# Kernel tuning notes

Hardware: AMD Instinct MI355X
Metric: run time of the kernel (lower is better)

Reference implementation:

```python
import jax, jax.numpy as jnp
import numpy as np

B, N, C, H, K = 16, 1024, 384, 6, 8
HID = int(C * 2.0)  # mlp_ratio = 2.0
HD = C // H


def _layernorm(x, w, b, eps=1e-5):
    m = x.mean(-1, keepdims=True)
    v = ((x - m) ** 2).mean(-1, keepdims=True)
    return (x - m) * jax.lax.rsqrt(v + eps) * w + b


def setup_inputs() -> dict:
    key = jax.random.key(0)
    ks = jax.random.split(key, 16)
    x = jax.random.normal(ks[0], (B, N, C), jnp.float32)
    # knn indices within each batch, offset by batch*N (as in get_knn_index)
    idx = jax.random.randint(ks[1], (B, K, N), 0, N)
    base = jnp.arange(B, dtype=jnp.int32)[:, None, None] * N
    knn_index = (idx + base).reshape(-1).astype(jnp.int32)
    s = 0.02
    p = {
        "x": x,
        "knn_index": knn_index,
        "ln1_w": jnp.ones((C,), jnp.float32),
        "ln1_b": jnp.zeros((C,), jnp.float32),
        "w_qkv": jax.random.normal(ks[2], (C, 3 * C), jnp.float32) * s,  # qkv_bias=False
        "w_proj": jax.random.normal(ks[3], (C, C), jnp.float32) * s,
        "b_proj": jnp.zeros((C,), jnp.float32),
        "w_knn": jax.random.normal(ks[4], (2 * C, C), jnp.float32) * s,
        "b_knn": jnp.zeros((C,), jnp.float32),
        "w_merge": jax.random.normal(ks[5], (2 * C, C), jnp.float32) * s,
        "b_merge": jnp.zeros((C,), jnp.float32),
        "ln2_w": jnp.ones((C,), jnp.float32),
        "ln2_b": jnp.zeros((C,), jnp.float32),
        "w_fc1": jax.random.normal(ks[6], (C, HID), jnp.float32) * s,
        "b_fc1": jnp.zeros((HID,), jnp.float32),
        "w_fc2": jax.random.normal(ks[7], (HID, C), jnp.float32) * s,
        "b_fc2": jnp.zeros((C,), jnp.float32),
    }
    return p


def reference(x, knn_index, ln1_w, ln1_b, w_qkv, w_proj, b_proj, w_knn, b_knn,
              w_merge, b_merge, ln2_w, ln2_b, w_fc1, b_fc1, w_fc2, b_fc2):
    nx = _layernorm(x, ln1_w, ln1_b)  # [B,N,C]

    # --- self attention ---
    qkv = (nx @ w_qkv).reshape(B, N, 3, H, HD)
    q, k, v = qkv[:, :, 0], qkv[:, :, 1], qkv[:, :, 2]  # [B,N,H,HD]
    scale = HD ** (-0.5)
    attn = jnp.einsum("bnhd,bmhd->bhnm", q, k) * scale
    attn = jax.nn.softmax(attn, axis=-1)
    a_out = jnp.einsum("bhnm,bmhd->bnhd", attn, v).reshape(B, N, C)
    x1 = a_out @ w_proj + b_proj

    # --- graph feature: gather, relative concat, Linear+LeakyReLU, max over k ---
    feat = nx.reshape(B * N, C)[knn_index].reshape(B, K, N, C)
    center = nx[:, None, :, :]  # [B,1,N,C]
    g = jnp.concatenate([feat - center, jnp.broadcast_to(center, (B, K, N, C))], axis=-1)
    knn_f = jax.nn.leaky_relu(g @ w_knn + b_knn, negative_slope=0.2)
    knn_f = knn_f.max(axis=1)  # [B,N,C]

    x1 = jnp.concatenate([x1, knn_f], axis=-1) @ w_merge + b_merge
    x = x + x1

    # --- MLP ---
    h = _layernorm(x, ln2_w, ln2_b)
    h = jax.nn.gelu(h @ w_fc1 + b_fc1, approximate=False) @ w_fc2 + b_fc2
    return x + h
```

## Files before the change

kernel.cpp:

```cpp
#include <hip/hip_runtime.h>
#include <hip/hip_bf16.h>
#include <math.h>

#define BN_ROWS 16384
#define CDIM 384
#define NH 6
#define BBATCH 16
#define NNN 1024

typedef unsigned short u16;
typedef unsigned int u32;
typedef __attribute__((ext_vector_type(8))) short short8;
typedef __attribute__((ext_vector_type(4))) float floatx4;

__device__ __forceinline__ float b2f(u16 s) { return __uint_as_float(((u32)s) << 16); }
__device__ __forceinline__ u16 f2b(float f) {
    __hip_bfloat16 h = __float2bfloat16(f);
    u16 s; __builtin_memcpy(&s, &h, 2); return s;
}
__device__ __forceinline__ u32 cvt_pk_bf16(float lo, float hi) {
    u32 r;
    asm("v_cvt_pk_bf16_f32 %0, %1, %2" : "=v"(r) : "v"(lo), "v"(hi));
    return r;
}
__device__ __forceinline__ void gload_lds16(const u16* g, u16* l) {
    __builtin_amdgcn_global_load_lds(
        (const __attribute__((address_space(1))) unsigned int*)g,
        (__attribute__((address_space(3))) unsigned int*)l, 16, 0, 0);
}

__global__ __launch_bounds__(256) void pack_all(
    const float* __restrict__ W0, u16* __restrict__ T0,
    const float* __restrict__ W1, u16* __restrict__ T1,
    const float* __restrict__ W2, u16* __restrict__ T2,
    const float* __restrict__ W3, u16* __restrict__ T3,
    const float* __restrict__ W4, u16* __restrict__ T4,
    const float* __restrict__ W5, u16* __restrict__ T5)
{
    const float* W; u16* T; int K, N;
    switch (blockIdx.z) {
        case 0: W = W0; T = T0; K = 384; N = 1152; break;
        case 1: W = W1; T = T1; K = 384; N = 384;  break;
        case 2: W = W2; T = T2; K = 768; N = 384;  break;
        case 3: W = W3; T = T3; K = 768; N = 384;  break;
        case 4: W = W4; T = T4; K = 384; N = 768;  break;
        default: W = W5; T = T5; K = 768; N = 384; break;
    }
    const int n0 = blockIdx.x * 32, k0 = blockIdx.y * 32;
    if (n0 >= N || k0 >= K) return;
    __shared__ float s[32][33];
    const int tx = threadIdx.x & 31, ty = threadIdx.x >> 5;
#pragma unroll
    for (int i = 0; i < 4; ++i)
        s[ty + 8 * i][tx] = W[(size_t)(k0 + ty + 8 * i) * N + n0 + tx];
    __syncthreads();
#pragma unroll
    for (int i = 0; i < 4; ++i)
        T[(size_t)(n0 + ty + 8 * i) * K + k0 + tx] = f2b(s[tx][ty + 8 * i]);
}

__global__ __launch_bounds__(64) void ln_kernel(const float* __restrict__ xin,
                                                const float* __restrict__ w,
                                                const float* __restrict__ b,
                                                u16* __restrict__ out)
{
    const int row = blockIdx.x;
    const int t = threadIdx.x;
    const size_t base = (size_t)row * CDIM;
    float v[6];
#pragma unroll
    for (int i = 0; i < 6; ++i) v[i] = xin[base + t + 64 * i];
    float s = 0.f, s2 = 0.f;
#pragma unroll
    for (int i = 0; i < 6; ++i) { s += v[i]; s2 += v[i] * v[i]; }
#pragma unroll
    for (int m = 1; m < 64; m <<= 1) {
        s  += __shfl_xor(s,  m, 64);
        s2 += __shfl_xor(s2, m, 64);
    }
    const float mean = s * (1.0f / CDIM);
    const float var  = s2 * (1.0f / CDIM) - mean * mean;
    const float rs   = rsqrtf(var + 1e-5f);
#pragma unroll
    for (int i = 0; i < 6; ++i) {
        int c = t + 64 * i;
        out[base + c] = f2b((v[i] - mean) * rs * w[c] + b[c]);
    }
}

template<int ACT, bool HAS_BIAS, bool HAS_RES, bool OUT_F32, int MODE, int NT, bool SWZ>
__global__ __launch_bounds__(256) void gemm_mfma_kernel(
    const u16* __restrict__ A, int lda,
    const u16* __restrict__ Bt, const u16* __restrict__ Bt2, int ldbt,
    u16* Cb, u16* Cb2, u16* Cb3, float* Cf, int ldc,
    const float* __restrict__ bias,
    const float* res,
    int K)
{
    constexpr int NTL = NT / 32;
    __shared__ u16 As[2][128 * 32];
    __shared__ u16 Bs[2][NT * 32];
    const int tid  = threadIdx.x;
    const int wv   = tid >> 6;
    const int lane = tid & 63;
    const int l15  = lane & 15;
    const int quad = lane >> 4;

    int m0, n0;
    if (SWZ) {
        const int nbx = gridDim.x;
        const int total = nbx * gridDim.y;
        int lin = blockIdx.x + nbx * blockIdx.y;
        const int cpx = total >> 3;
        lin = (lin & 7) * cpx + (lin >> 3);
        m0 = (lin / nbx) * 128;
        n0 = (lin % nbx) * NT;
    } else {
        m0 = blockIdx.y * 128;
        n0 = blockIdx.x * NT;
    }

    const int woffm = (wv >> 1) * 64;
    const int woffn = (wv & 1) * (NT / 2);

    const u16* bsrc; int brow0, koff, bld;
    if constexpr (MODE == 3) {
        if (n0 < 1152)      { bsrc = Bt;  brow0 = n0;        koff = 0;   bld = 384; }
        else if (n0 < 1536) { bsrc = Bt2; brow0 = n0 - 1152; koff = 0;   bld = 768; }
        else                { bsrc = Bt2; brow0 = n0 - 1536; koff = 384; bld = 768; }
    } else {
        bsrc  = (MODE == 2 && n0 >= 384) ? Bt2 : Bt;
        brow0 = (MODE == 2 && n0 >= 384) ? (n0 - 384) : n0;
        koff = 0; bld = ldbt;
    }

    floatx4 acc[4][NTL];
#pragma unroll
    for (int mt = 0; mt < 4; ++mt)
#pragma unroll
        for (int nt = 0; nt < NTL; ++nt) acc[mt][nt] = (floatx4){0.f, 0.f, 0.f, 0.f};

    const int gsw  = 8 * ((lane & 3) ^ ((lane >> 3) & 3));
    const int rloc = lane >> 2;
    const int rdsw = 8 * (quad ^ ((l15 >> 1) & 3));

    auto stage = [&](int kt, int p) {
#pragma unroll
        for (int j = 0; j < 2; ++j) {
            const int slab = 32 * wv + 16 * j;
            gload_lds16(A + (size_t)(m0 + slab + rloc) * lda + kt + gsw, &As[p][slab * 32]);
        }
        if (NT == 128) {
#pragma unroll
            for (int j = 0; j < 2; ++j) {
                const int slab = 32 * wv + 16 * j;
                gload_lds16(bsrc + (size_t)(brow0 + slab + rloc) * bld + koff + kt + gsw,
                            &Bs[p][slab * 32]);
            }
        } else {
            const int slab = 16 * wv;
            gload_lds16(bsrc + (size_t)(brow0 + slab + rloc) * bld + koff + kt + gsw,
                        &Bs[p][slab * 32]);
        }
    };

    stage(0, 0);
    stage(32, 1);
    int cur = 0;
    for (int kt = 0; kt < K; kt += 32) {
        if (kt + 32 < K) {
            if constexpr (NT == 128) asm volatile("s_waitcnt vmcnt(4)" ::: "memory");
            else                     asm volatile("s_waitcnt vmcnt(3)" ::: "memory");
        } else {
            asm volatile("s_waitcnt vmcnt(0)" ::: "memory");
        }
        __builtin_amdgcn_sched_barrier(0);
        __builtin_amdgcn_s_barrier();
        __builtin_amdgcn_sched_barrier(0);

        short8 af[4], bf[NTL];
#pragma unroll
        for (int mt = 0; mt < 4; ++mt)
            af[mt] = *(const short8*)(As[cur] + (woffm + mt * 16 + l15) * 32 + rdsw);
#pragma unroll
        for (int nt = 0; nt < NTL; ++nt)
            bf[nt] = *(const short8*)(Bs[cur] + (woffn + nt * 16 + l15) * 32 + rdsw);
#pragma unroll
        for (int mt = 0; mt < 4; ++mt)
#pragma unroll
            for (int nt = 0; nt < NTL; ++nt)
                acc[mt][nt] = __builtin_amdgcn_mfma_f32_16x16x32_bf16(
                    bf[nt], af[mt], acc[mt][nt], 0, 0, 0);
        __builtin_amdgcn_sched_barrier(0);
        __builtin_amdgcn_s_barrier();
        __builtin_amdgcn_sched_barrier(0);
        if (kt + 64 < K) stage(kt + 64, cur);
        cur ^= 1;
    }

#pragma unroll
    for (int mt = 0; mt < 4; ++mt) {
        const int gr = m0 + woffm + mt * 16 + l15;
#pragma unroll
        for (int nt = 0; nt < NTL; ++nt) {
            const int gc0 = n0 + woffn + nt * 16 + quad * 4;
            float v4[4];
#pragma unroll
            for (int rr = 0; rr < 4; ++rr) v4[rr] = acc[mt][nt][rr];
            if (HAS_BIAS) {
                const floatx4 bv = *(const floatx4*)(bias + gc0);
#pragma unroll
                for (int rr = 0; rr < 4; ++rr) v4[rr] += bv[rr];
            }
            if (MODE == 2 && gc0 >= 384) {
                const floatx4 bv = *(const floatx4*)(bias + gc0 - 384);
#pragma unroll
                for (int rr = 0; rr < 4; ++rr) v4[rr] += bv[rr];
            }
            if (MODE == 3 && gc0 >= 1536) {
                const floatx4 bv = *(const floatx4*)(bias + gc0 - 1536);
#pragma unroll
                for (int rr = 0; rr < 4; ++rr) v4[rr] += bv[rr];
            }
            if (ACT == 1) {
#pragma unroll
                for (int rr = 0; rr < 4; ++rr)
                    v4[rr] = 0.5f * v4[rr] * (1.0f + erff(v4[rr] * 0.70710678118654752f));
            }
            if (HAS_RES) {
                const floatx4 rv = *(const floatx4*)(res + (size_t)gr * ldc + gc0);
#pragma unroll
                for (int rr = 0; rr < 4; ++rr) v4[rr] += rv[rr];
            }
            if (MODE == 1 || (MODE == 3 && gc0 < 1152)) {
                const int t3  = gc0 / 384;
                const int rem = gc0 - t3 * 384;
                const int hh = rem >> 6, dd = rem & 63;
                const int bb = gr >> 10, nn = gr & 1023;
                u32 lo = cvt_pk_bf16(v4[0], v4[1]);
                u32 hi = cvt_pk_bf16(v4[2], v4[3]);
                *(uint2*)(Cb + ((size_t)((bb * 6 + hh) * 1024 + nn)) * 192 + t3 * 64 + dd) =
                    make_uint2(lo, hi);
            } else if (MODE == 3) {
                u32 lo = cvt_pk_bf16(v4[0], v4[1]);
                u32 hi = cvt_pk_bf16(v4[2], v4[3]);
                if (gc0 < 1536)
                    *(uint2*)(Cb2 + (size_t)gr * 384 + gc0 - 1152) = make_uint2(lo, hi);
                else
                    *(uint2*)(Cb3 + (size_t)gr * 384 + gc0 - 1536) = make_uint2(lo, hi);
            } else if (MODE == 2) {
                u32 lo = cvt_pk_bf16(v4[0], v4[1]);
                u32 hi = cvt_pk_bf16(v4[2], v4[3]);
                if (gc0 < 384)
                    *(uint2*)(Cb  + (size_t)gr * 384 + gc0)       = make_uint2(lo, hi);
                else
                    *(uint2*)(Cb2 + (size_t)gr * 384 + gc0 - 384) = make_uint2(lo, hi);
            } else if (OUT_F32) {
                floatx4 vv = {v4[0], v4[1], v4[2], v4[3]};
                *(floatx4*)(Cf + (size_t)gr * ldc + gc0) = vv;
            } else {
                u32 lo = cvt_pk_bf16(v4[0], v4[1]);
                u32 hi = cvt_pk_bf16(v4[2], v4[3]);
                *(uint2*)(Cb + (size_t)gr * ldc + gc0) = make_uint2(lo, hi);
            }
        }
    }
}

__global__ __launch_bounds__(256) void attn_mfma_kernel(const u16* __restrict__ qkv2,
                                                        u16* __restrict__ aout)
{
    const int id = blockIdx.x;
    const int rxcd = id & 7;
    const int j = id >> 3;
    const int slab = rxcd + 8 * (j % 12);
    const int qtile = j / 12;
    const int b = slab / NH, h = slab % NH;

    const int wave = threadIdx.x >> 6;
    const int lane = threadIdx.x & 63;
    const int l15 = lane & 15;
    const int quad = lane >> 4;
    const int qbase = qtile * 128 + wave * 32;
    const int tid = threadIdx.x;

    const u16* slabp = qkv2 + ((size_t)(b * NH + h) << 10) * 192;

    __shared__ __align__(16) u16 Ks[64 * 72];
    __shared__ __align__(16) u16 Vt[64 * 72];
    __shared__ __align__(16) u16 Ps[4][32 * 72];

    short8 qf[2][2];
#pragma unroll
    for (int nt = 0; nt < 2; ++nt) {
        const u16* qrow = slabp + (size_t)(qbase + nt * 16 + l15) * 192;
        qf[nt][0] = *(const short8*)(qrow + quad * 8);
        qf[nt][1] = *(const short8*)(qrow + 32 + quad * 8);
    }

    short8 vones;
#pragma unroll
    for (int i = 0; i < 8; ++i) vones[i] = (l15 == 0) ? (short)0x3F80 : (short)0;

    floatx4 Oacc[2][4];
    floatx4 rAcc[2];
#pragma unroll
    for (int mt = 0; mt < 2; ++mt) {
        rAcc[mt] = (floatx4){0.f, 0.f, 0.f, 0.f};
#pragma unroll
        for (int nt = 0; nt < 4; ++nt) Oacc[mt][nt] = (floatx4){0.f, 0.f, 0.f, 0.f};
    }

    const int key = tid >> 2, dblk = (tid & 3) * 16;
    const int kp2 = tid & 31, db = (tid >> 5) * 8;
    uint4 kr0, kr1, vr0, vr1;
    {
        const u16* kp = slabp + (size_t)key * 192 + 64 + dblk;
        kr0 = *(const uint4*)(kp);
        kr1 = *(const uint4*)(kp + 8);
        const u16* vp = slabp + (size_t)(2 * kp2) * 192 + 128 + db;
        vr0 = *(const uint4*)(vp);
        vr1 = *(const uint4*)(vp + 192);
    }

    for (int kc = 0; kc < NNN; kc += 64) {
        *(uint4*)(Ks + key * 72 + dblk)     = kr0;
        *(uint4*)(Ks + key * 72 + dblk + 8) = kr1;
        {
            u32 a0[4] = {vr0.x, vr0.y, vr0.z, vr0.w};
            u32 a1[4] = {vr1.x, vr1.y, vr1.z, vr1.w};
#pragma unroll
            for (int i = 0; i < 4; ++i) {
                u32 lo = __builtin_amdgcn_perm(a1[i], a0[i], 0x05040100u);
                u32 hi = __builtin_amdgcn_perm(a1[i], a0[i], 0x07060302u);
                *(u32*)(Vt + (size_t)(db + 2 * i)     * 72 + 2 * kp2) = lo;
                *(u32*)(Vt + (size_t)(db + 2 * i + 1) * 72 + 2 * kp2) = hi;
            }
        }
        __syncthreads();

        if (kc + 64 < NNN) {
            const u16* kp = slabp + (size_t)(kc + 64 + key) * 192 + 64 + dblk;
            kr0 = *(const uint4*)(kp);
            kr1 = *(const uint4*)(kp + 8);
            const u16* vp = slabp + (size_t)(kc + 64 + 2 * kp2) * 192 + 128 + db;
            vr0 = *(const uint4*)(vp);
            vr1 = *(const uint4*)(vp + 192);
        }

        floatx4 sc[4][2];
        __builtin_amdgcn_s_setprio(1);
#pragma unroll
        for (int kt_ = 0; kt_ < 4; ++kt_) {
            short8 kf0 = *(const short8*)(Ks + (kt_ * 16 + l15) * 72 + quad * 8);
            short8 kf1 = *(const short8*)(Ks + (kt_ * 16 + l15) * 72 + 32 + quad * 8);
#pragma unroll
            for (int nt = 0; nt < 2; ++nt) {
                floatx4 s = {0.f, 0.f, 0.f, 0.f};
                s = __builtin_amdgcn_mfma_f32_16x16x32_bf16(kf0, qf[nt][0], s, 0, 0, 0);
                s = __builtin_amdgcn_mfma_f32_16x16x32_bf16(kf1, qf[nt][1], s, 0, 0, 0);
                sc[kt_][nt] = s;
            }
        }
        __builtin_amdgcn_s_setprio(0);

#pragma unroll
        for (int kt_ = 0; kt_ < 4; ++kt_)
#pragma unroll
            for (int nt = 0; nt < 2; ++nt) {
                float pv[4];
#pragma unroll
                for (int rr = 0; rr < 4; ++rr)
                    pv[rr] = __expf(sc[kt_][nt][rr] * 0.125f);
                u32 lo = cvt_pk_bf16(pv[0], pv[1]);
                u32 hi = cvt_pk_bf16(pv[2], pv[3]);
                *(uint2*)(Ps[wave] + (nt * 16 + l15) * 72 + kt_ * 16 + quad * 4) =
                    make_uint2(lo, hi);
            }

        short8 pf[2][2];
#pragma unroll
        for (int mt = 0; mt < 2; ++mt) {
            pf[mt][0] = *(const short8*)(Ps[wave] + (mt * 16 + l15) * 72 + quad * 8);
            pf[mt][1] = *(const short8*)(Ps[wave] + (mt * 16 + l15) * 72 + 32 + quad * 8);
        }
        __builtin_amdgcn_s_setprio(1);
#pragma unroll
        for (int mt = 0; mt < 2; ++mt) {
            rAcc[mt] = __builtin_amdgcn_mfma_f32_16x16x32_bf16(pf[mt][0], vones, rAcc[mt], 0, 0, 0);
            rAcc[mt] = __builtin_amdgcn_mfma_f32_16x16x32_bf16(pf[mt][1], vones, rAcc[mt], 0, 0, 0);
        }
#pragma unroll
        for (int nt = 0; nt < 4; ++nt) {
#pragma unroll
            for (int kk = 0; kk < 2; ++kk) {
                short8 vf = *(const short8*)(Vt + (size_t)(nt * 16 + l15) * 72 + kk * 32 + quad * 8);
#pragma unroll
                for (int mt = 0; mt < 2; ++mt)
                    Oacc[mt][nt] = __builtin_amdgcn_mfma_f32_16x16x32_bf16(
                        pf[mt][kk], vf, Oacc[mt][nt], 0, 0, 0);
            }
        }
        __builtin_amdgcn_s_setprio(0);
        __syncthreads();
    }

#pragma unroll
    for (int mt = 0; mt < 2; ++mt) {
#pragma unroll
        for (int rr = 0; rr < 4; ++rr) {
            float l = __shfl(rAcc[mt][rr], quad << 4, 64);
            float inv = 1.0f / l;
            int q = qbase + mt * 16 + quad * 4 + rr;
#pragma unroll
            for (int nt = 0; nt < 4; ++nt)
                aout[(size_t)(b * NNN + q) * CDIM + h * 64 + nt * 16 + l15] =
                    f2b(Oacc[mt][nt][rr] * inv);
        }
    }
}

__global__ __launch_bounds__(128) void knnmax_kernel(const u16* __restrict__ t1,
                                                     const u16* __restrict__ t2,
                                                     const int* __restrict__ idx,
                                                     u16* __restrict__ x1cat)
{
    const int bn = blockIdx.x * 2 + (threadIdx.x >> 6);
    const int lane = threadIdx.x & 63;
    if (lane >= 48) return;
    const int b = bn >> 10, n = bn & 1023;
    int ind[8];
#pragma unroll
    for (int k = 0; k < 8; ++k) ind[k] = idx[b * 8192 + k * 1024 + n];
    const int c0 = lane * 8;
    const size_t rbase = (size_t)bn * CDIM + c0;
    short8 v1 = *(const short8*)(t1 + rbase);
    short8 v2 = *(const short8*)(t2 + rbase);
    float basef[8], mx[8];
#pragma unroll
    for (int j = 0; j < 8; ++j) {
        basef[j] = b2f((u16)v2[j]) - b2f((u16)v1[j]);
        mx[j] = -1e30f;
    }
#pragma unroll
    for (int k = 0; k < 8; ++k) {
        short8 nv = *(const short8*)(t1 + (size_t)ind[k] * CDIM + c0);
#pragma unroll
        for (int j = 0; j < 8; ++j) {
            float v = b2f((u16)nv[j]) + basef[j];
            v = (v > 0.f) ? v : 0.2f * v;
            mx[j] = fmaxf(mx[j], v);
        }
    }
    short8 ov;
#pragma unroll
    for (int j = 0; j < 8; ++j) ov[j] = (short)f2b(mx[j]);
    *(short8*)(x1cat + (size_t)bn * 768 + CDIM + c0) = ov;
}

extern "C" void kernel_launch(void* const* d_in, const int* in_sizes, int n_in,
                              void* d_out, int out_size, void* d_ws, size_t ws_size,
                              hipStream_t stream)
{
    (void)in_sizes; (void)n_in; (void)out_size; (void)ws_size;
    const float* x     = (const float*)d_in[0];
    const int*   knn   = (const int*)d_in[1];
    const float* ln1w  = (const float*)d_in[2];
    const float* ln1b  = (const float*)d_in[3];
    const float* wqkv  = (const float*)d_in[4];
    const float* wproj = (const float*)d_in[5];
    const float* bproj = (const float*)d_in[6];
    const float* wknn  = (const float*)d_in[7];
    const float* bknn  = (const float*)d_in[8];
    const float* wmrg  = (const float*)d_in[9];
    const float* bmrg  = (const float*)d_in[10];
    const float* ln2w  = (const float*)d_in[11];
    const float* ln2b  = (const float*)d_in[12];
    const float* wfc1  = (const float*)d_in[13];
    const float* bfc1  = (const float*)d_in[14];
    const float* wfc2  = (const float*)d_in[15];
    const float* bfc2  = (const float*)d_in[16];

    u16* wsb = (u16*)d_ws;
    const size_t RE = (size_t)BN_ROWS * CDIM;
    u16* nxb   = wsb;
    u16* qkvb  = wsb + RE;
    u16* aoutb = wsb;
    u16* x1cat = wsb + RE;
    u16* hinb  = wsb;
    u16* h1b   = wsb + RE;
    u16* t1b   = (u16*)d_out;
    u16* t2b   = (u16*)d_out + RE;
    float* xmid = (float*)d_out;
    u16* wqkvT  = wsb + 4 * RE;
    u16* wprojT = wqkvT + 442368;
    u16* wknnT  = wprojT + 147456;
    u16* wmrgT  = wknnT + 294912;
    u16* wfc1T  = wmrgT + 294912;
    u16* wfc2T  = wfc1T + 294912;

    pack_all<<<dim3(36, 24, 6), 256, 0, stream>>>(
        wqkv, wqkvT, wproj, wprojT, wknn, wknnT, wmrg, wmrgT, wfc1, wfc1T, wfc2, wfc2T);
    ln_kernel<<<BN_ROWS, 64, 0, stream>>>(x, ln1w, ln1b, nxb);
    gemm_mfma_kernel<0, false, false, false, 3, 128, true><<<dim3(15, 128), 256, 0, stream>>>(
        nxb, CDIM, wqkvT, wknnT, 384, qkvb, t1b, t2b, nullptr, 0, bknn, nullptr, CDIM);
    attn_mfma_kernel<<<768, 256, 0, stream>>>(qkvb, aoutb);
    gemm_mfma_kernel<0, true, false, false, 0, 64, true><<<dim3(6, 128), 256, 0, stream>>>(
        aoutb, CDIM, wprojT, nullptr, CDIM, x1cat, nullptr, nullptr, nullptr, 768, bproj, nullptr, CDIM);
    knnmax_kernel<<<BN_ROWS / 2, 128, 0, stream>>>(t1b, t2b, knn, x1cat);
    gemm_mfma_kernel<0, true, true, true, 0, 64, true><<<dim3(6, 128), 256, 0, stream>>>(
        x1cat, 768, wmrgT, nullptr, 768, nullptr, nullptr, nullptr, xmid, CDIM, bmrg, x, 768);
    ln_kernel<<<BN_ROWS, 64, 0, stream>>>(xmid, ln2w, ln2b, hinb);
    gemm_mfma_kernel<1, true, false, false, 0, 128, true><<<dim3(6, 128), 256, 0, stream>>>(
        hinb, CDIM, wfc1T, nullptr, CDIM, h1b, nullptr, nullptr, nullptr, 768, bfc1, nullptr, CDIM);
    gemm_mfma_kernel<0, true, true, true, 0, 64, true><<<dim3(6, 128), 256, 0, stream>>>(
        h1b, 768, wfc2T, nullptr, 768, nullptr, nullptr, nullptr, (float*)d_out, CDIM, bfc2, xmid, 768);
}
```

Measured before the change: 306.1 us.

## Load GEMM MFMA fragments directly from global memory, dropping LDS staging

Result: slower. 498.2 us (+62.8%).

```diff
diff --git a/kernel.cpp b/kernel.cpp
--- a/kernel.cpp
+++ b/kernel.cpp
@@ -22,11 +22,6 @@
     u32 r;
     asm("v_cvt_pk_bf16_f32 %0, %1, %2" : "=v"(r) : "v"(lo), "v"(hi));
     return r;
-}
-__device__ __forceinline__ void gload_lds16(const u16* g, u16* l) {
-    __builtin_amdgcn_global_load_lds(
-        (const __attribute__((address_space(1))) unsigned int*)g,
-        (__attribute__((address_space(3))) unsigned int*)l, 16, 0, 0);
 }
 
 __global__ __launch_bounds__(256) void pack_all(
@@ -98,8 +93,6 @@
     int K)
 {
     constexpr int NTL = NT / 32;
-    __shared__ u16 As[2][128 * 32];
-    __shared__ u16 Bs[2][NT * 32];
     const int tid  = threadIdx.x;
     const int wv   = tid >> 6;
     const int lane = tid & 63;
@@ -140,63 +133,38 @@
 #pragma unroll
         for (int nt = 0; nt < NTL; ++nt) acc[mt][nt] = (floatx4){0.f, 0.f, 0.f, 0.f};
 
-    const int gsw  = 8 * ((lane & 3) ^ ((lane >> 3) & 3));
-    const int rloc = lane >> 2;
-    const int rdsw = 8 * (quad ^ ((l15 >> 1) & 3));
-
-    auto stage = [&](int kt, int p) {
-#pragma unroll
-        for (int j = 0; j < 2; ++j) {
-            const int slab = 32 * wv + 16 * j;
-            gload_lds16(A + (size_t)(m0 + slab + rloc) * lda + kt + gsw, &As[p][slab * 32]);
-        }
-        if (NT == 128) {
-#pragma unroll
-            for (int j = 0; j < 2; ++j) {
-                const int slab = 32 * wv + 16 * j;
-                gload_lds16(bsrc + (size_t)(brow0 + slab + rloc) * bld + koff + kt + gsw,
-                            &Bs[p][slab * 32]);
-            }
-        } else {
-            const int slab = 16 * wv;
-            gload_lds16(bsrc + (size_t)(brow0 + slab + rloc) * bld + koff + kt + gsw,
-                        &Bs[p][slab * 32]);
-        }
-    };
-
-    stage(0, 0);
-    stage(32, 1);
-    int cur = 0;
-    for (int kt = 0; kt < K; kt += 32) {
-        if (kt + 32 < K) {
-            if constexpr (NT == 128) asm volatile("s_waitcnt vmcnt(4)" ::: "memory");
-            else                     asm volatile("s_waitcnt vmcnt(3)" ::: "memory");
-        } else {
-            asm volatile("s_waitcnt vmcnt(0)" ::: "memory");
-        }
-        __builtin_amdgcn_sched_barrier(0);
-        __builtin_amdgcn_s_barrier();
-        __builtin_amdgcn_sched_barrier(0);
-
-        short8 af[4], bf[NTL];
-#pragma unroll
-        for (int mt = 0; mt < 4; ++mt)
-            af[mt] = *(const short8*)(As[cur] + (woffm + mt * 16 + l15) * 32 + rdsw);
-#pragma unroll
-        for (int nt = 0; nt < NTL; ++nt)
-            bf[nt] = *(const short8*)(Bs[cur] + (woffn + nt * 16 + l15) * 32 + rdsw);
-#pragma unroll
-        for (int mt = 0; mt < 4; ++mt)
-#pragma unroll
-            for (int nt = 0; nt < NTL; ++nt)
-                acc[mt][nt] = __builtin_amdgcn_mfma_f32_16x16x32_bf16(
-                    bf[nt], af[mt], acc[mt][nt], 0, 0, 0);
-        __builtin_amdgcn_sched_barrier(0);
-        __builtin_amdgcn_s_barrier();
-        __builtin_amdgcn_sched_barrier(0);
-        if (kt + 64 < K) stage(kt + 64, cur);
-        cur ^= 1;
-    }
+    const u16* Ab = A    + (size_t)(m0 + woffm + l15) * lda + quad * 8;
+    const u16* Bb = bsrc + (size_t)(brow0 + woffn + l15) * bld + koff + quad * 8;
+
+#define LDFRAG(kt, af, bf)                                                       \
+    {                                                                            \
+        _Pragma("unroll")                                                        \
+        for (int mt = 0; mt < 4; ++mt)                                           \
+            af[mt] = *(const short8*)(Ab + (size_t)mt * 16 * lda + (kt));        \
+        _Pragma("unroll")                                                        \
+        for (int nt = 0; nt < NTL; ++nt)                                         \
+            bf[nt] = *(const short8*)(Bb + (size_t)nt * 16 * bld + (kt));        \
+    }
+#define DOMFMA(af, bf)                                                           \
+    {                                                                            \
+        _Pragma("unroll")                                                        \
+        for (int mt = 0; mt < 4; ++mt)                                           \
+            _Pragma("unroll")                                                    \
+            for (int nt = 0; nt < NTL; ++nt)                                     \
+                acc[mt][nt] = __builtin_amdgcn_mfma_f32_16x16x32_bf16(           \
+                    bf[nt], af[mt], acc[mt][nt], 0, 0, 0);                       \
+    }
+
+    short8 af0[4], bf0[NTL], af1[4], bf1[NTL];
+    LDFRAG(0, af0, bf0);
+    for (int kt = 0; kt < K; kt += 64) {
+        LDFRAG(kt + 32, af1, bf1);
+        DOMFMA(af0, bf0);
+        if (kt + 64 < K) LDFRAG(kt + 64, af0, bf0);
+        DOMFMA(af1, bf1);
+    }
+#undef LDFRAG
+#undef DOMFMA
 
 #pragma unroll
     for (int mt = 0; mt < 4; ++mt) {
@@ -502,7 +470,7 @@
     pack_all<<<dim3(36, 24, 6), 256, 0, stream>>>(
         wqkv, wqkvT, wproj, wprojT, wknn, wknnT, wmrg, wmrgT, wfc1, wfc1T, wfc2, wfc2T);
     ln_kernel<<<BN_ROWS, 64, 0, stream>>>(x, ln1w, ln1b, nxb);
-    gemm_mfma_kernel<0, false, false, false, 3, 128, true><<<dim3(15, 128), 256, 0, stream>>>(
+    gemm_mfma_kernel<0, false, false, false, 3, 64, true><<<dim3(30, 128), 256, 0, stream>>>(
         nxb, CDIM, wqkvT, wknnT, 384, qkvb, t1b, t2b, nullptr, 0, bknn, nullptr, CDIM);
     attn_mfma_kernel<<<768, 256, 0, stream>>>(qkvb, aoutb);
     gemm_mfma_kernel<0, true, false, false, 0, 64, true><<<dim3(6, 128), 256, 0, stream>>>(
@@ -511,7 +479,7 @@
     gemm_mfma_kernel<0, true, true, true, 0, 64, true><<<dim3(6, 128), 256, 0, stream>>>(
         x1cat, 768, wmrgT, nullptr, 768, nullptr, nullptr, nullptr, xmid, CDIM, bmrg, x, 768);
     ln_kernel<<<BN_ROWS, 64, 0, stream>>>(xmid, ln2w, ln2b, hinb);
-    gemm_mfma_kernel<1, true, false, false, 0, 128, true><<<dim3(6, 128), 256, 0, stream>>>(
+    gemm_mfma_kernel<1, true, false, false, 0, 64, true><<<dim3(12, 128), 256, 0, stream>>>(
         hinb, CDIM, wfc1T, nullptr, CDIM, h1b, nullptr, nullptr, nullptr, 768, bfc1, nullptr, CDIM);
     gemm_mfma_kernel<0, true, true, true, 0, 64, true><<<dim3(6, 128), 256, 0, stream>>>(
         h1b, 768, wfc2T, nullptr, 768, nullptr, nullptr, nullptr, (float*)d_out, CDIM, bfc2, xmid, 768);
```

## Merge projection GEMM and kNN max-gather into one heterogeneous launch

Applied to the files above, without the earlier changes.

New measurement: 296.4 us, median of 2. 3.1% less time.

```diff
diff --git a/kernel.cpp b/kernel.cpp
--- a/kernel.cpp
+++ b/kernel.cpp
@@ -267,6 +267,132 @@
     }
 }
 
+__global__ __launch_bounds__(256) void projknn_kernel(
+    const u16* __restrict__ A,
+    const u16* __restrict__ Bt,
+    const float* __restrict__ bias,
+    const u16* __restrict__ t1,
+    const u16* __restrict__ t2,
+    const int* __restrict__ idx,
+    u16* __restrict__ x1cat)
+{
+    constexpr int GB = 768;
+    __shared__ u16 As[2][128 * 32];
+    __shared__ u16 Bs[2][64 * 32];
+    const int tid  = threadIdx.x;
+    const int lane = tid & 63;
+
+    if (blockIdx.x >= GB) {
+        const int bn = (blockIdx.x - GB) * 4 + (tid >> 6);
+        if (lane >= 48) return;
+        const int b = bn >> 10, n = bn & 1023;
+        int ind[8];
+#pragma unroll
+        for (int k = 0; k < 8; ++k) ind[k] = idx[b * 8192 + k * 1024 + n];
+        const int c0 = lane * 8;
+        const size_t rbase = (size_t)bn * CDIM + c0;
+        short8 v1 = *(const short8*)(t1 + rbase);
+        short8 v2 = *(const short8*)(t2 + rbase);
+        float basef[8], mx[8];
+#pragma unroll
+        for (int j = 0; j < 8; ++j) {
+            basef[j] = b2f((u16)v2[j]) - b2f((u16)v1[j]);
+            mx[j] = -1e30f;
+        }
+#pragma unroll
+        for (int k = 0; k < 8; ++k) {
+            short8 nv = *(const short8*)(t1 + (size_t)ind[k] * CDIM + c0);
+#pragma unroll
+            for (int j = 0; j < 8; ++j) {
+                float v = b2f((u16)nv[j]) + basef[j];
+                v = (v > 0.f) ? v : 0.2f * v;
+                mx[j] = fmaxf(mx[j], v);
+            }
+        }
+        short8 ov;
+#pragma unroll
+        for (int j = 0; j < 8; ++j) ov[j] = (short)f2b(mx[j]);
+        *(short8*)(x1cat + (size_t)bn * 768 + CDIM + c0) = ov;
+        return;
+    }
+
+    const int wv   = tid >> 6;
+    const int l15  = lane & 15;
+    const int quad = lane >> 4;
+    int lin = blockIdx.x;
+    lin = (lin & 7) * 96 + (lin >> 3);
+    const int m0 = (lin / 6) * 128;
+    const int n0 = (lin % 6) * 64;
+    const int woffm = (wv >> 1) * 64;
+    const int woffn = (wv & 1) * 32;
+
+    floatx4 acc[4][2];
+#pragma unroll
+    for (int mt = 0; mt < 4; ++mt)
+#pragma unroll
+        for (int nt = 0; nt < 2; ++nt) acc[mt][nt] = (floatx4){0.f, 0.f, 0.f, 0.f};
+
+    const int gsw  = 8 * ((lane & 3) ^ ((lane >> 3) & 3));
+    const int rloc = lane >> 2;
+    const int rdsw = 8 * (quad ^ ((l15 >> 1) & 3));
+
+    auto stage = [&](int kt, int p) {
+#pragma unroll
+        for (int j = 0; j < 2; ++j) {
+            const int slab = 32 * wv + 16 * j;
+            gload_lds16(A + (size_t)(m0 + slab + rloc) * CDIM + kt + gsw, &As[p][slab * 32]);
+        }
+        const int slab = 16 * wv;
+        gload_lds16(Bt + (size_t)(n0 + slab + rloc) * CDIM + kt + gsw, &Bs[p][slab * 32]);
+    };
+
+    stage(0, 0);
+    stage(32, 1);
+    int cur = 0;
+    for (int kt = 0; kt < CDIM; kt += 32) {
+        if (kt + 32 < CDIM) asm volatile("s_waitcnt vmcnt(3)" ::: "memory");
+        else                asm volatile("s_waitcnt vmcnt(0)" ::: "memory");
+        __builtin_amdgcn_sched_barrier(0);
+        __builtin_amdgcn_s_barrier();
+        __builtin_amdgcn_sched_barrier(0);
+
+        short8 af[4], bf[2];
+#pragma unroll
+        for (int mt = 0; mt < 4; ++mt)
+            af[mt] = *(const short8*)(As[cur] + (woffm + mt * 16 + l15) * 32 + rdsw);
+#pragma unroll
+        for (int nt = 0; nt < 2; ++nt)
+            bf[nt] = *(const short8*)(Bs[cur] + (woffn + nt * 16 + l15) * 32 + rdsw);
+#pragma unroll
+        for (int mt = 0; mt < 4; ++mt)
+#pragma unroll
+            for (int nt = 0; nt < 2; ++nt)
+                acc[mt][nt] = __builtin_amdgcn_mfma_f32_16x16x32_bf16(
+                    bf[nt], af[mt], acc[mt][nt], 0, 0, 0);
+        __builtin_amdgcn_sched_barrier(0);
+        __builtin_amdgcn_s_barrier();
+        __builtin_amdgcn_sched_barrier(0);
+        if (kt + 64 < CDIM) stage(kt + 64, cur);
+        cur ^= 1;
+    }
+
+#pragma unroll
+    for (int mt = 0; mt < 4; ++mt) {
+        const int gr = m0 + woffm + mt * 16 + l15;
+#pragma unroll
+        for (int nt = 0; nt < 2; ++nt) {
+            const int gc0 = n0 + woffn + nt * 16 + quad * 4;
+            const floatx4 bv = *(const floatx4*)(bias + gc0);
+            float v4[4];
+#pragma unroll
+            for (int rr = 0; rr < 4; ++rr) v4[rr] = acc[mt][nt][rr] + bv[rr];
+            u32 lo = cvt_pk_bf16(v4[0], v4[1]);
+            u32 hi = cvt_pk_bf16(v4[2], v4[3]);
+            *(uint2*)(x1cat + (size_t)gr * 768 + gc0) = make_uint2(lo, hi);
+        }
+    }
+}
+
 __global__ __launch_bounds__(256) void attn_mfma_kernel(const u16* __restrict__ qkv2,
                                                         u16* __restrict__ aout)
 {
@@ -418,44 +544,6 @@
                     f2b(Oacc[mt][nt][rr] * inv);
         }
     }
-}
-
-__global__ __launch_bounds__(128) void knnmax_kernel(const u16* __restrict__ t1,
-                                                     const u16* __restrict__ t2,
-                                                     const int* __restrict__ idx,
-                                                     u16* __restrict__ x1cat)
-{
-    const int bn = blockIdx.x * 2 + (threadIdx.x >> 6);
-    const int lane = threadIdx.x & 63;
-    if (lane >= 48) return;
-    const int b = bn >> 10, n = bn & 1023;
-    int ind[8];
-#pragma unroll
-    for (int k = 0; k < 8; ++k) ind[k] = idx[b * 8192 + k * 1024 + n];
-    const int c0 = lane * 8;
-    const size_t rbase = (size_t)bn * CDIM + c0;
-    short8 v1 = *(const short8*)(t1 + rbase);
-    short8 v2 = *(const short8*)(t2 + rbase);
-    float basef[8], mx[8];
-#pragma unroll
-    for (int j = 0; j < 8; ++j) {
-        basef[j] = b2f((u16)v2[j]) - b2f((u16)v1[j]);
-        mx[j] = -1e30f;
-    }
-#pragma unroll
-    for (int k = 0; k < 8; ++k) {
-        short8 nv = *(const short8*)(t1 + (size_t)ind[k] * CDIM + c0);
-#pragma unroll
-        for (int j = 0; j < 8; ++j) {
-            float v = b2f((u16)nv[j]) + basef[j];
-            v = (v > 0.f) ? v : 0.2f * v;
-            mx[j] = fmaxf(mx[j], v);
-        }
-    }
-    short8 ov;
-#pragma unroll
-    for (int j = 0; j < 8; ++j) ov[j] = (short)f2b(mx[j]);
-    *(short8*)(x1cat + (size_t)bn * 768 + CDIM + c0) = ov;
 }
 
 extern "C" void kernel_launch(void* const* d_in, const int* in_sizes, int n_in,
@@ -505,9 +593,8 @@
     gemm_mfma_kernel<0, false, false, false, 3, 128, true><<<dim3(15, 128), 256, 0, stream>>>(
         nxb, CDIM, wqkvT, wknnT, 384, qkvb, t1b, t2b, nullptr, 0, bknn, nullptr, CDIM);
     attn_mfma_kernel<<<768, 256, 0, stream>>>(qkvb, aoutb);
-    gemm_mfma_kernel<0, true, false, false, 0, 64, true><<<dim3(6, 128), 256, 0, stream>>>(
-        aoutb, CDIM, wprojT, nullptr, CDIM, x1cat, nullptr, nullptr, nullptr, 768, bproj, nullptr, CDIM);
-    knnmax_kernel<<<BN_ROWS / 2, 128, 0, stream>>>(t1b, t2b, knn, x1cat);
+    projknn_kernel<<<768 + BN_ROWS / 4, 256, 0, stream>>>(
+        aoutb, wprojT, bproj, t1b, t2b, knn, x1cat);
     gemm_mfma_kernel<0, true, true, true, 0, 64, true><<<dim3(6, 128), 256, 0, stream>>>(
         x1cat, 768, wmrgT, nullptr, 768, nullptr, nullptr, nullptr, xmid, CDIM, bmrg, x, 768);
     ln_kernel<<<BN_ROWS, 64, 0, stream>>>(xmid, ln2w, ln2b, hinb);
```
